# Performance work log

Hardware: AMD Instinct MI355X
Metric: run time of the kernel (lower is better)

The kernel has to match this reference:

```python
import jax, jax.numpy as jnp
import numpy as np

B, L, D, E, K, DFF = 2, 2048, 1024, 8, 2, 4096


def setup_inputs() -> dict:
    key = jax.random.key(0)
    kx, kr, kg, ku, kd = jax.random.split(key, 5)
    scale = 0.02
    return {
        "x": jax.random.normal(kx, (B, L, D), dtype=jnp.float32),
        "Wr": jax.random.normal(kr, (E, D), dtype=jnp.float32) * scale,   # router: logits = x @ Wr.T
        "Wg": jax.random.normal(kg, (E, DFF, D), dtype=jnp.float32) * scale,  # gate proj per expert
        "Wu": jax.random.normal(ku, (E, DFF, D), dtype=jnp.float32) * scale,  # up proj per expert
        "Wd": jax.random.normal(kd, (E, D, DFF), dtype=jnp.float32) * scale,  # down proj per expert
    }


def reference(x, Wr, Wg, Wu, Wd):
    Bb, Ll, Dd = x.shape
    T = Bb * Ll
    xt = x.reshape(T, Dd)                                   # [T, D]
    logits = jnp.einsum("td,ed->te", xt, Wr)                # router logits [T, E]
    scores = jax.nn.softmax(logits, axis=-1)
    k_scores, k_ids = jax.lax.top_k(scores, K)              # [T, K]
    eps = jnp.finfo(x.dtype).eps
    k_w = k_scores / (k_scores.sum(axis=-1, keepdims=True) + eps)  # renormalized top-k weights
    # combine[t, e] = sum_k k_w[t, k] * (k_ids[t, k] == e)
    combine = jnp.sum(jax.nn.one_hot(k_ids, E, dtype=x.dtype) * k_w[..., None], axis=1)  # [T, E]
    # GluMLP per expert, computed densely over all tokens (reference form)
    g = jnp.einsum("td,efd->etf", xt, Wg)                   # [E, T, DFF]
    u = jnp.einsum("td,efd->etf", xt, Wu)                   # [E, T, DFF]
    h = jax.nn.relu(g) * u
    out_e = jnp.einsum("etf,edf->etd", h, Wd)               # [E, T, D]
    out = jnp.einsum("te,etd->td", combine, out_e)          # weighted combine [T, D]
    return out.reshape(Bb, Ll, Dd)
```

## Files before the change

### kernel.cpp

```cpp
#include <hip/hip_runtime.h>
#include <hip/hip_bf16.h>

#define Tt 4096
#define Dd 1024
#define Ee 8
#define Kk 2
#define Ff 4096

using f32x4  = __attribute__((ext_vector_type(4))) float;
using bf16x8 = __attribute__((ext_vector_type(8))) short;

__device__ __forceinline__ unsigned short f2bf(float f) {
    union { float fp; unsigned int u; } v; v.fp = f;
    unsigned int u = v.u;
    return (unsigned short)((u + 0x7FFFu + ((u >> 16) & 1u)) >> 16);
}

__device__ __forceinline__ void gl16(const void* g, void* l) {
    __builtin_amdgcn_global_load_lds(
        (const __attribute__((address_space(1))) void*)g,
        (__attribute__((address_space(3))) void*)l, 16, 0, 0);
}

__global__ void router_kernel(const float* __restrict__ x, const float* __restrict__ Wr,
                              int* __restrict__ ids, float* __restrict__ wts,
                              int* __restrict__ counts, unsigned short* __restrict__ xb) {
    const int t = blockIdx.x;
    const int lane = threadIdx.x;
    const float* xr = x + (size_t)t * Dd + lane * 16;
    float xv[16];
#pragma unroll
    for (int i = 0; i < 4; ++i) *(float4*)(xv + 4 * i) = *(const float4*)(xr + 4 * i);
    uint4 o0, o1;
    o0.x = (unsigned)f2bf(xv[0])  | ((unsigned)f2bf(xv[1])  << 16);
    o0.y = (unsigned)f2bf(xv[2])  | ((unsigned)f2bf(xv[3])  << 16);
    o0.z = (unsigned)f2bf(xv[4])  | ((unsigned)f2bf(xv[5])  << 16);
    o0.w = (unsigned)f2bf(xv[6])  | ((unsigned)f2bf(xv[7])  << 16);
    o1.x = (unsigned)f2bf(xv[8])  | ((unsigned)f2bf(xv[9])  << 16);
    o1.y = (unsigned)f2bf(xv[10]) | ((unsigned)f2bf(xv[11]) << 16);
    o1.z = (unsigned)f2bf(xv[12]) | ((unsigned)f2bf(xv[13]) << 16);
    o1.w = (unsigned)f2bf(xv[14]) | ((unsigned)f2bf(xv[15]) << 16);
    unsigned short* xo = xb + (size_t)t * Dd + lane * 16;
    *(uint4*)(xo) = o0;
    *(uint4*)(xo + 8) = o1;

    double dot[Ee];
#pragma unroll
    for (int e = 0; e < Ee; ++e) {
        const float* wr = Wr + e * Dd + lane * 16;
        double s = 0.0;
#pragma unroll
        for (int i = 0; i < 16; ++i) s += (double)xv[i] * (double)wr[i];
        dot[e] = s;
    }
#pragma unroll
    for (int off = 32; off >= 1; off >>= 1) {
#pragma unroll
        for (int e = 0; e < Ee; ++e) dot[e] += __shfl_xor(dot[e], off, 64);
    }
    if (lane == 0) {
        float lg[Ee];
#pragma unroll
        for (int e = 0; e < Ee; ++e) lg[e] = (float)dot[e];
        float m = lg[0];
        for (int e = 1; e < Ee; ++e) m = fmaxf(m, lg[e]);
        float ex[Ee]; float sum = 0.f;
        for (int e = 0; e < Ee; ++e) { ex[e] = expf(lg[e] - m); sum += ex[e]; }
        float s0 = -1.f, s1 = -1.f; int i0 = 0, i1 = 0;
        for (int e = 0; e < Ee; ++e) {
            float s = ex[e];
            if (s > s0)      { s1 = s0; i1 = i0; s0 = s; i0 = e; }
            else if (s > s1) { s1 = s; i1 = e; }
        }
        float inv = 1.f / sum;
        float sc0 = s0 * inv, sc1 = s1 * inv;
        float den = sc0 + sc1 + 1.1920929e-7f;
        ids[2 * t] = i0; ids[2 * t + 1] = i1;
        wts[2 * t] = sc0 / den; wts[2 * t + 1] = sc1 / den;
        atomicAdd(&counts[i0], 1);
        atomicAdd(&counts[i1], 1);
    }
}

__global__ void cvt_wgu(const float* __restrict__ Wg, const float* __restrict__ Wu,
                        unsigned short* __restrict__ Wgu) {
    size_t tid = (size_t)blockIdx.x * blockDim.x + threadIdx.x;
    size_t row = tid >> 7;
    int dc  = (int)(tid & 127);
    int e   = (int)(row >> 13);
    int j   = (int)(row & 8191);
    int fg = j >> 5, s = (j >> 4) & 1, fi = j & 15;
    int f  = fg * 16 + fi;
    const float* src = (s ? Wu : Wg) + ((size_t)e * Ff + f) * Dd + dc * 8;
    float4 a = *(const float4*)(src);
    float4 b = *(const float4*)(src + 4);
    uint4 o;
    o.x = (unsigned)f2bf(a.x) | ((unsigned)f2bf(a.y) << 16);
    o.y = (unsigned)f2bf(a.z) | ((unsigned)f2bf(a.w) << 16);
    o.z = (unsigned)f2bf(b.x) | ((unsigned)f2bf(b.y) << 16);
    o.w = (unsigned)f2bf(b.z) | ((unsigned)f2bf(b.w) << 16);
    *(uint4*)(Wgu + row * Dd + dc * 8) = o;
}

__global__ void scan_kernel(const int* __restrict__ counts, int* __restrict__ cursor,
                            int* __restrict__ eoff) {
    if (threadIdx.x == 0) {
        int acc = 0;
        for (int e = 0; e < Ee; ++e) { eoff[e] = acc; cursor[e] = acc; acc += counts[e]; }
        eoff[Ee] = acc;
    }
}

__global__ void scatter_kernel(const int* __restrict__ ids,
                               int* __restrict__ cursor, int* __restrict__ rows) {
    int t = blockIdx.x * blockDim.x + threadIdx.x;
    if (t >= Tt) return;
#pragma unroll
    for (int k = 0; k < Kk; ++k) {
        int e = ids[2 * t + k];
        int pos = atomicAdd(&cursor[e], 1);
        rows[pos] = 2 * t + k;
    }
}


#define MFMA_BF16(a, b, c) __builtin_amdgcn_mfma_f32_16x16x32_bf16(a, b, c, 0, 0, 0)

template<bool G2>
__device__ __forceinline__ void gemm_body(unsigned short* Ls,
                                          const unsigned short* __restrict__ Abase,
                                          const unsigned short* __restrict__ Bbase,
                                          const int* __restrict__ eoff,
                                          const int* __restrict__ rows,
                                          unsigned short* __restrict__ H,
                                          float* __restrict__ partial) {
    constexpr int KLEN  = G2 ? Ff : Dd;
    constexpr int NT    = (G2 ? 2048 : 1024) / 64;
    constexpr int MT    = G2 ? 128 : 256;
    constexpr int MFR   = MT / 32;
    constexpr int AISS  = MT / 64;
    constexpr int AH0   = AISS / 2;
    constexpr int ABUFU = MT * 64;
    constexpr int BBASE = 2 * ABUFU;
    const int e   = blockIdx.z;
    const int off = eoff[e];
    const int ne  = eoff[e + 1] - off;
    const int by  = blockIdx.y;
    const int my  = G2 ? (by >> 1) : by;
    const int sK  = G2 ? (by & 1) : 0;
    const int koff = sK * 2048;
    const int m0  = my * MT;
    if (m0 >= ne) return;
    const int n0  = blockIdx.x * 256;

    const int tid  = threadIdx.x;
    const int lane = tid & 63;
    const int w    = tid >> 6;
    const int wr   = w >> 2;
    const int wc   = w & 3;
    const int lr   = lane & 15;
    const int lc   = lane >> 4;

    const int sr = lane >> 3;
    const int cA = (lane & 7) ^ sr;
    int asrc[AISS];
#pragma unroll
    for (int j = 0; j < AISS; ++j) {
        int rr = m0 + j * 64 + w * 8 + sr;
        if (rr > ne - 1) rr = ne - 1;
        asrc[j] = (G2 ? (off + rr) : (rows[off + rr] >> 1)) * KLEN + cA * 8;
    }
    const unsigned short* Bp = Bbase + (size_t)e * (G2 ? (size_t)Dd * Ff : (size_t)8192 * Dd);
    int bsrc[4];
#pragma unroll
    for (int qq = 0; qq < 4; ++qq) {
        int rN = n0 + qq * 64 + w * 8 + sr;
        bsrc[qq] = rN * KLEN + cA * 8;
    }

    auto STAGE_A = [&](int T, int half) {
        const int bo_ = (T & 1) * ABUFU; const int kt_ = koff + T * 64;
        if (half == 0) {
#pragma unroll
            for (int j = 0; j < AH0; ++j)
                gl16(Abase + asrc[j] + kt_, Ls + bo_ + j * 4096 + w * 512);
        } else {
#pragma unroll
            for (int j = AH0; j < AISS; ++j)
                gl16(Abase + asrc[j] + kt_, Ls + bo_ + j * 4096 + w * 512);
        }
    };
    auto STAGE_B = [&](int T, int Hh) {
        const int bo_ = BBASE + (T & 1) * 16384; const int kt_ = koff + T * 64;
        gl16(Bp + bsrc[2 * Hh]     + kt_, Ls + bo_ + (2 * Hh)     * 4096 + w * 512);
        gl16(Bp + bsrc[2 * Hh + 1] + kt_, Ls + bo_ + (2 * Hh + 1) * 4096 + w * 512);
    };

#define WAIT_STEADY() do { if constexpr (G2) { asm volatile("s_waitcnt vmcnt(2)" ::: "memory"); } \
                           else              { asm volatile("s_waitcnt vmcnt(4)" ::: "memory"); } } while (0)

    const int ccx0 = ((0 * 4 + lc) ^ (lr & 7)) * 8;
    const int ccx1 = ((1 * 4 + lc) ^ (lr & 7)) * 8;
    const int aB = (wr * (MT / 2)) * 64 + lr * 64;
    const int bB = BBASE + wc * 4096 + lr * 64;

    f32x4 acc[MFR][4];
#pragma unroll
    for (int m = 0; m < MFR; ++m)
#pragma unroll
        for (int n = 0; n < 4; ++n) acc[m][n] = (f32x4){0.f, 0.f, 0.f, 0.f};

    STAGE_A(0, 0); STAGE_A(0, 1); STAGE_B(0, 0); STAGE_B(0, 1);
    STAGE_A(1, 0); STAGE_A(1, 1);
    WAIT_STEADY();
    __builtin_amdgcn_sched_barrier(0);
    __builtin_amdgcn_s_barrier();

    bf16x8 a0[MFR], a1[MFR], b0[4], b1[4];

    for (int t = 0; t < NT; ++t) {
        const int abo = (t & 1) * ABUFU;
        const int bbo = (t & 1) * 16384;
#pragma unroll
        for (int m = 0; m < MFR; ++m) a0[m] = *(const bf16x8*)(Ls + abo + aB + m * 1024 + ccx0);
#pragma unroll
        for (int n = 0; n < 4; ++n) b0[n] = *(const bf16x8*)(Ls + bbo + bB + n * 1024 + ccx0);
        if (t + 1 < NT) STAGE_B(t + 1, 0);
        __builtin_amdgcn_s_barrier();
        asm volatile("s_waitcnt lgkmcnt(0)" ::: "memory");
        __builtin_amdgcn_sched_barrier(0);
        __builtin_amdgcn_s_setprio(1);
#pragma unroll
        for (int m = 0; m < MFR; ++m) {
            acc[m][0] = MFMA_BF16(a0[m], b0[0], acc[m][0]);
            acc[m][1] = MFMA_BF16(a0[m], b0[1], acc[m][1]);
        }
        __builtin_amdgcn_s_setprio(0);
        __builtin_amdgcn_s_barrier();
#pragma unroll
        for (int m = 0; m < MFR; ++m) a1[m] = *(const bf16x8*)(Ls + abo + aB + m * 1024 + ccx1);
        if (t + 1 < NT) STAGE_B(t + 1, 1);
        __builtin_amdgcn_s_barrier();
        __builtin_amdgcn_s_setprio(1);
#pragma unroll
        for (int m = 0; m < MFR; ++m) {
            acc[m][2] = MFMA_BF16(a0[m], b0[2], acc[m][2]);
            acc[m][3] = MFMA_BF16(a0[m], b0[3], acc[m][3]);
        }
        __builtin_amdgcn_s_setprio(0);
        asm volatile("s_waitcnt lgkmcnt(0)" ::: "memory");
        __builtin_amdgcn_sched_barrier(0);
        __builtin_amdgcn_s_barrier();
#pragma unroll
        for (int n = 0; n < 4; ++n) b1[n] = *(const bf16x8*)(Ls + bbo + bB + n * 1024 + ccx1);
        if (t + 2 < NT) STAGE_A(t + 2, 0);
        __builtin_amdgcn_s_barrier();
        asm volatile("s_waitcnt lgkmcnt(0)" ::: "memory");
        __builtin_amdgcn_sched_barrier(0);
        __builtin_amdgcn_s_setprio(1);
#pragma unroll
        for (int m = 0; m < MFR; ++m) {
            acc[m][0] = MFMA_BF16(a1[m], b1[0], acc[m][0]);
            acc[m][1] = MFMA_BF16(a1[m], b1[1], acc[m][1]);
        }
        __builtin_amdgcn_s_setprio(0);
        __builtin_amdgcn_s_barrier();
        if (t + 2 < NT) STAGE_A(t + 2, 1);
        __builtin_amdgcn_s_setprio(1);
#pragma unroll
        for (int m = 0; m < MFR; ++m) {
            acc[m][2] = MFMA_BF16(a1[m], b1[2], acc[m][2]);
            acc[m][3] = MFMA_BF16(a1[m], b1[3], acc[m][3]);
        }
        __builtin_amdgcn_s_setprio(0);
        if (t + 2 < NT) { WAIT_STEADY(); }
        else            { asm volatile("s_waitcnt vmcnt(0)" ::: "memory"); }
        __builtin_amdgcn_sched_barrier(0);
        __builtin_amdgcn_s_barrier();
    }

    if constexpr (!G2) {
        const int fg16 = ((n0 + wc * 64) >> 5) * 16 + lr;
#pragma unroll
        for (int m = 0; m < MFR; ++m) {
            const int itok = m0 + wr * (MT / 2) + m * 16 + lc * 4;
#pragma unroll
            for (int r = 0; r < 4; ++r) {
                const int i = itok + r;
                if (i < ne) {
                    unsigned short* hp = H + (size_t)(off + i) * Ff;
#pragma unroll
                    for (int np = 0; np < 2; ++np) {
                        const float g = acc[m][2 * np][r];
                        const float u = acc[m][2 * np + 1][r];
                        hp[fg16 + np * 16] = f2bf(fmaxf(g, 0.f) * u);
                    }
                }
            }
        }
    } else {
        const int dbase = n0 + wc * 64;
#pragma unroll
        for (int m = 0; m < MFR; ++m) {
            const int ib = m0 + wr * (MT / 2) + m * 16 + lc * 4;
#pragma unroll
            for (int r = 0; r < 4; ++r) {
                const int i = ib + r;
                if (i < ne) {
                    const int tr = rows[off + i];
                    float* op = partial + ((size_t)sK * 8192 + tr) * Dd + dbase + lr;
#pragma unroll
                    for (int n = 0; n < 4; ++n) op[n * 16] = acc[m][n][r];
                }
            }
        }
    }
#undef WAIT_STEADY
}

__global__ __launch_bounds__(512, 1)
void g1_moe(const unsigned short* __restrict__ xb, const unsigned short* __restrict__ Wgu,
            const int* __restrict__ eoff, const int* __restrict__ rows,
            unsigned short* __restrict__ H,
            const float* __restrict__ Wd, unsigned short* __restrict__ Wdb) {
    __shared__ __align__(16) unsigned short Ls[65536];
    gemm_body<false>(Ls, xb, Wgu, eoff, rows, H, nullptr);
    const int fb = blockIdx.x + gridDim.x * (blockIdx.y + gridDim.y * blockIdx.z);
    const size_t base = (size_t)fb * 8192;
#pragma unroll
    for (int it = 0; it < 2; ++it) {
        const size_t i = base + (size_t)it * 4096 + threadIdx.x * 8;
        float4 a = *(const float4*)(Wd + i);
        float4 b = *(const float4*)(Wd + i + 4);
        uint4 o;
        o.x = (unsigned)f2bf(a.x) | ((unsigned)f2bf(a.y) << 16);
        o.y = (unsigned)f2bf(a.z) | ((unsigned)f2bf(a.w) << 16);
        o.z = (unsigned)f2bf(b.x) | ((unsigned)f2bf(b.y) << 16);
        o.w = (unsigned)f2bf(b.z) | ((unsigned)f2bf(b.w) << 16);
        *(uint4*)(Wdb + i) = o;
    }
}

__global__ __launch_bounds__(512, 1)
void g2_moe(const unsigned short* __restrict__ H, const unsigned short* __restrict__ Wdb,
            const int* __restrict__ eoff, const int* __restrict__ rows,
            float* __restrict__ partial) {
    __shared__ __align__(16) unsigned short Ls[49152];
    gemm_body<true>(Ls, H, Wdb, eoff, rows, nullptr, partial);
}

__global__ void reduce_kernel(const float* __restrict__ P, const float* __restrict__ wts,
                              float* __restrict__ out) {
    const size_t idx = (size_t)blockIdx.x * blockDim.x + threadIdx.x;
    const size_t t  = idx >> 8;
    const int   dq  = (int)(idx & 255);
    const float w0 = wts[2 * t], w1 = wts[2 * t + 1];
    const float4* p00 = (const float4*)(P + (2 * t)        * Dd) + dq;
    const float4* p01 = (const float4*)(P + (2 * t + 1)    * Dd) + dq;
    const float4* p10 = (const float4*)(P + ((size_t)8192 + 2 * t)     * Dd) + dq;
    const float4* p11 = (const float4*)(P + ((size_t)8192 + 2 * t + 1) * Dd) + dq;
    float4 a = *p00, b = *p01, c = *p10, d = *p11;
    float4 o;
    o.x = w0 * (a.x + c.x) + w1 * (b.x + d.x);
    o.y = w0 * (a.y + c.y) + w1 * (b.y + d.y);
    o.z = w0 * (a.z + c.z) + w1 * (b.z + d.z);
    o.w = w0 * (a.w + c.w) + w1 * (b.w + d.w);
    ((float4*)(out + t * Dd))[dq] = o;
}

extern "C" void kernel_launch(void* const* d_in, const int* in_sizes, int n_in,
                              void* d_out, int out_size, void* d_ws, size_t ws_size,
                              hipStream_t stream) {
    const float* x  = (const float*)d_in[0];
    const float* Wr = (const float*)d_in[1];
    const float* Wg = (const float*)d_in[2];
    const float* Wu = (const float*)d_in[3];
    const float* Wd = (const float*)d_in[4];
    float* out = (float*)d_out;
    char* ws = (char*)d_ws;

    const size_t WELEM    = (size_t)Ee * Ff * Dd;
    const size_t OFF_IDS  = 256;
    const size_t OFF_WTS  = OFF_IDS  + (size_t)Tt * 2 * 4;
    const size_t OFF_ROWS = OFF_WTS  + (size_t)Tt * 2 * 4;
    const size_t OFF_ROWW = OFF_ROWS + (size_t)Tt * Kk * 4;
    const size_t OFF_XB   = OFF_ROWW + (size_t)Tt * Kk * 4;
    const size_t OFF_H    = OFF_XB   + (size_t)Tt * Dd * 2;
    const size_t OFF_WGU  = OFF_H    + (size_t)Tt * Kk * Ff * 2;
    const size_t OFF_WD   = OFF_WGU  + WELEM * 2 * 2;
    const size_t NEED     = OFF_WD   + WELEM * 2;
    if (ws_size < NEED) return;

    int* counts = (int*)ws;
    int* cursor = (int*)(ws + 32);
    int* eoff   = (int*)(ws + 64);
    int* ids    = (int*)(ws + OFF_IDS);
    float* wts  = (float*)(ws + OFF_WTS);
    int* rows   = (int*)(ws + OFF_ROWS);
    unsigned short* xb  = (unsigned short*)(ws + OFF_XB);
    unsigned short* H   = (unsigned short*)(ws + OFF_H);
    unsigned short* Wgu = (unsigned short*)(ws + OFF_WGU);
    unsigned short* Wdb = (unsigned short*)(ws + OFF_WD);
    float* partial = (float*)(ws + OFF_WGU);

    hipMemsetAsync(ws, 0, 256, stream);

    router_kernel  <<<Tt, 64, 0, stream>>>(x, Wr, ids, wts, counts, xb);
    scan_kernel    <<<1, 64, 0, stream>>>(counts, cursor, eoff);
    scatter_kernel <<<Tt / 256, 256, 0, stream>>>(ids, cursor, rows);

    cvt_wgu        <<<32768, 256, 0, stream>>>(Wg, Wu, Wgu);

    g1_moe <<<dim3(2 * Ff / 256, Tt / 256, Ee), 512, 0, stream>>>(
        xb, Wgu, eoff, rows, H, Wd, Wdb);
    g2_moe <<<dim3(Dd / 256, 20, Ee), 512, 0, stream>>>(
        H, Wdb, eoff, rows, partial);

    reduce_kernel  <<<(Tt * Dd / 4) / 256, 256, 0, stream>>>(partial, wts, out);
}
```

Before: 494.8 us.

## Narrow g2 N-tile to 128 and store split-K partials as bf16

The down-projection GEMM now uses a 128-wide N tile instead of 256. That doubles the grid in x and cuts LDS to 64KB, giving more blocks to fill the CUs. The split-K partial sums are written as bf16 instead of fp32, which halves the partial write and reduce traffic; the reduce kernel is rewritten to read bf16x8 vectors. The cost is less B-operand reuse per block and extra rounding error from storing the partial results in bf16.

```diff
diff --git a/kernel.cpp b/kernel.cpp
--- a/kernel.cpp
+++ b/kernel.cpp
@@ -14,6 +14,10 @@
     union { float fp; unsigned int u; } v; v.fp = f;
     unsigned int u = v.u;
     return (unsigned short)((u + 0x7FFFu + ((u >> 16) & 1u)) >> 16);
+}
+
+__device__ __forceinline__ float b2f(unsigned short u) {
+    union { float f; unsigned int i; } v; v.i = (unsigned)u << 16; return v.f;
 }
 
 __device__ __forceinline__ void gl16(const void* g, void* l) {
@@ -133,14 +137,19 @@
                                           const int* __restrict__ eoff,
                                           const int* __restrict__ rows,
                                           unsigned short* __restrict__ H,
-                                          float* __restrict__ partial) {
+                                          unsigned short* __restrict__ partial) {
     constexpr int KLEN  = G2 ? Ff : Dd;
     constexpr int NT    = (G2 ? 2048 : 1024) / 64;
     constexpr int MT    = G2 ? 128 : 256;
+    constexpr int BN    = G2 ? 128 : 256;
     constexpr int MFR   = MT / 32;
+    constexpr int NF    = BN / 64;
     constexpr int AISS  = MT / 64;
+    constexpr int BISS  = BN / 64;
     constexpr int AH0   = AISS / 2;
+    constexpr int BH0   = BISS / 2;
     constexpr int ABUFU = MT * 64;
+    constexpr int BBUFU = BN * 64;
     constexpr int BBASE = 2 * ABUFU;
     const int e   = blockIdx.z;
     const int off = eoff[e];
@@ -151,7 +160,7 @@
     const int koff = sK * 2048;
     const int m0  = my * MT;
     if (m0 >= ne) return;
-    const int n0  = blockIdx.x * 256;
+    const int n0  = blockIdx.x * BN;
 
     const int tid  = threadIdx.x;
     const int lane = tid & 63;
@@ -171,11 +180,11 @@
         asrc[j] = (G2 ? (off + rr) : (rows[off + rr] >> 1)) * KLEN + cA * 8;
     }
     const unsigned short* Bp = Bbase + (size_t)e * (G2 ? (size_t)Dd * Ff : (size_t)8192 * Dd);
-    int bsrc[4];
-#pragma unroll
-    for (int qq = 0; qq < 4; ++qq) {
-        int rN = n0 + qq * 64 + w * 8 + sr;
-        bsrc[qq] = rN * KLEN + cA * 8;
+    int bsrc[BISS];
+#pragma unroll
+    for (int j = 0; j < BISS; ++j) {
+        int rN = n0 + j * 64 + w * 8 + sr;
+        bsrc[j] = rN * KLEN + cA * 8;
     }
 
     auto STAGE_A = [&](int T, int half) {
@@ -190,10 +199,17 @@
                 gl16(Abase + asrc[j] + kt_, Ls + bo_ + j * 4096 + w * 512);
         }
     };
-    auto STAGE_B = [&](int T, int Hh) {
-        const int bo_ = BBASE + (T & 1) * 16384; const int kt_ = koff + T * 64;
-        gl16(Bp + bsrc[2 * Hh]     + kt_, Ls + bo_ + (2 * Hh)     * 4096 + w * 512);
-        gl16(Bp + bsrc[2 * Hh + 1] + kt_, Ls + bo_ + (2 * Hh + 1) * 4096 + w * 512);
+    auto STAGE_B = [&](int T, int half) {
+        const int bo_ = BBASE + (T & 1) * BBUFU; const int kt_ = koff + T * 64;
+        if (half == 0) {
+#pragma unroll
+            for (int j = 0; j < BH0; ++j)
+                gl16(Bp + bsrc[j] + kt_, Ls + bo_ + j * 4096 + w * 512);
+        } else {
+#pragma unroll
+            for (int j = BH0; j < BISS; ++j)
+                gl16(Bp + bsrc[j] + kt_, Ls + bo_ + j * 4096 + w * 512);
+        }
     };
 
 #define WAIT_STEADY() do { if constexpr (G2) { asm volatile("s_waitcnt vmcnt(2)" ::: "memory"); } \
@@ -202,13 +218,13 @@
     const int ccx0 = ((0 * 4 + lc) ^ (lr & 7)) * 8;
     const int ccx1 = ((1 * 4 + lc) ^ (lr & 7)) * 8;
     const int aB = (wr * (MT / 2)) * 64 + lr * 64;
-    const int bB = BBASE + wc * 4096 + lr * 64;
-
-    f32x4 acc[MFR][4];
+    const int bB = BBASE + (wc * (BN / 4)) * 64 + lr * 64;
+
+    f32x4 acc[MFR][NF];
 #pragma unroll
     for (int m = 0; m < MFR; ++m)
 #pragma unroll
-        for (int n = 0; n < 4; ++n) acc[m][n] = (f32x4){0.f, 0.f, 0.f, 0.f};
+        for (int n = 0; n < NF; ++n) acc[m][n] = (f32x4){0.f, 0.f, 0.f, 0.f};
 
     STAGE_A(0, 0); STAGE_A(0, 1); STAGE_B(0, 0); STAGE_B(0, 1);
     STAGE_A(1, 0); STAGE_A(1, 1);
@@ -216,25 +232,25 @@
     __builtin_amdgcn_sched_barrier(0);
     __builtin_amdgcn_s_barrier();
 
-    bf16x8 a0[MFR], a1[MFR], b0[4], b1[4];
+    bf16x8 a0[MFR], a1[MFR], b0[NF], b1[NF];
 
     for (int t = 0; t < NT; ++t) {
         const int abo = (t & 1) * ABUFU;
-        const int bbo = (t & 1) * 16384;
+        const int bbo = (t & 1) * BBUFU;
 #pragma unroll
         for (int m = 0; m < MFR; ++m) a0[m] = *(const bf16x8*)(Ls + abo + aB + m * 1024 + ccx0);
 #pragma unroll
-        for (int n = 0; n < 4; ++n) b0[n] = *(const bf16x8*)(Ls + bbo + bB + n * 1024 + ccx0);
+        for (int n = 0; n < NF; ++n) b0[n] = *(const bf16x8*)(Ls + bbo + bB + n * 1024 + ccx0);
         if (t + 1 < NT) STAGE_B(t + 1, 0);
         __builtin_amdgcn_s_barrier();
         asm volatile("s_waitcnt lgkmcnt(0)" ::: "memory");
         __builtin_amdgcn_sched_barrier(0);
         __builtin_amdgcn_s_setprio(1);
 #pragma unroll
-        for (int m = 0; m < MFR; ++m) {
-            acc[m][0] = MFMA_BF16(a0[m], b0[0], acc[m][0]);
-            acc[m][1] = MFMA_BF16(a0[m], b0[1], acc[m][1]);
-        }
+        for (int m = 0; m < MFR; ++m)
+#pragma unroll
+            for (int n = 0; n < NF / 2; ++n)
+                acc[m][n] = MFMA_BF16(a0[m], b0[n], acc[m][n]);
         __builtin_amdgcn_s_setprio(0);
         __builtin_amdgcn_s_barrier();
 #pragma unroll
@@ -243,35 +259,35 @@
         __builtin_amdgcn_s_barrier();
         __builtin_amdgcn_s_setprio(1);
 #pragma unroll
-        for (int m = 0; m < MFR; ++m) {
-            acc[m][2] = MFMA_BF16(a0[m], b0[2], acc[m][2]);
-            acc[m][3] = MFMA_BF16(a0[m], b0[3], acc[m][3]);
-        }
+        for (int m = 0; m < MFR; ++m)
+#pragma unroll
+            for (int n = NF / 2; n < NF; ++n)
+                acc[m][n] = MFMA_BF16(a0[m], b0[n], acc[m][n]);
         __builtin_amdgcn_s_setprio(0);
         asm volatile("s_waitcnt lgkmcnt(0)" ::: "memory");
         __builtin_amdgcn_sched_barrier(0);
         __builtin_amdgcn_s_barrier();
 #pragma unroll
-        for (int n = 0; n < 4; ++n) b1[n] = *(const bf16x8*)(Ls + bbo + bB + n * 1024 + ccx1);
+        for (int n = 0; n < NF; ++n) b1[n] = *(const bf16x8*)(Ls + bbo + bB + n * 1024 + ccx1);
         if (t + 2 < NT) STAGE_A(t + 2, 0);
         __builtin_amdgcn_s_barrier();
         asm volatile("s_waitcnt lgkmcnt(0)" ::: "memory");
         __builtin_amdgcn_sched_barrier(0);
         __builtin_amdgcn_s_setprio(1);
 #pragma unroll
-        for (int m = 0; m < MFR; ++m) {
-            acc[m][0] = MFMA_BF16(a1[m], b1[0], acc[m][0]);
-            acc[m][1] = MFMA_BF16(a1[m], b1[1], acc[m][1]);
-        }
+        for (int m = 0; m < MFR; ++m)
+#pragma unroll
+            for (int n = 0; n < NF / 2; ++n)
+                acc[m][n] = MFMA_BF16(a1[m], b1[n], acc[m][n]);
         __builtin_amdgcn_s_setprio(0);
         __builtin_amdgcn_s_barrier();
         if (t + 2 < NT) STAGE_A(t + 2, 1);
         __builtin_amdgcn_s_setprio(1);
 #pragma unroll
-        for (int m = 0; m < MFR; ++m) {
-            acc[m][2] = MFMA_BF16(a1[m], b1[2], acc[m][2]);
-            acc[m][3] = MFMA_BF16(a1[m], b1[3], acc[m][3]);
-        }
+        for (int m = 0; m < MFR; ++m)
+#pragma unroll
+            for (int n = NF / 2; n < NF; ++n)
+                acc[m][n] = MFMA_BF16(a1[m], b1[n], acc[m][n]);
         __builtin_amdgcn_s_setprio(0);
         if (t + 2 < NT) { WAIT_STEADY(); }
         else            { asm volatile("s_waitcnt vmcnt(0)" ::: "memory"); }
@@ -299,7 +315,7 @@
             }
         }
     } else {
-        const int dbase = n0 + wc * 64;
+        const int dbase = n0 + wc * (BN / 4);
 #pragma unroll
         for (int m = 0; m < MFR; ++m) {
             const int ib = m0 + wr * (MT / 2) + m * 16 + lc * 4;
@@ -308,9 +324,9 @@
                 const int i = ib + r;
                 if (i < ne) {
                     const int tr = rows[off + i];
-                    float* op = partial + ((size_t)sK * 8192 + tr) * Dd + dbase + lr;
-#pragma unroll
-                    for (int n = 0; n < 4; ++n) op[n * 16] = acc[m][n][r];
+                    unsigned short* op = partial + ((size_t)sK * 8192 + tr) * Dd + dbase + lr;
+#pragma unroll
+                    for (int n = 0; n < NF; ++n) op[n * 16] = f2bf(acc[m][n][r]);
                 }
             }
         }
@@ -344,28 +360,33 @@
 __global__ __launch_bounds__(512, 1)
 void g2_moe(const unsigned short* __restrict__ H, const unsigned short* __restrict__ Wdb,
             const int* __restrict__ eoff, const int* __restrict__ rows,
-            float* __restrict__ partial) {
-    __shared__ __align__(16) unsigned short Ls[49152];
+            unsigned short* __restrict__ partial) {
+    __shared__ __align__(16) unsigned short Ls[32768];
     gemm_body<true>(Ls, H, Wdb, eoff, rows, nullptr, partial);
 }
 
-__global__ void reduce_kernel(const float* __restrict__ P, const float* __restrict__ wts,
+__global__ void reduce_kernel(const unsigned short* __restrict__ P, const float* __restrict__ wts,
                               float* __restrict__ out) {
     const size_t idx = (size_t)blockIdx.x * blockDim.x + threadIdx.x;
-    const size_t t  = idx >> 8;
-    const int   dq  = (int)(idx & 255);
+    const size_t t  = idx >> 7;
+    const int   dq  = (int)(idx & 127);
     const float w0 = wts[2 * t], w1 = wts[2 * t + 1];
-    const float4* p00 = (const float4*)(P + (2 * t)        * Dd) + dq;
-    const float4* p01 = (const float4*)(P + (2 * t + 1)    * Dd) + dq;
-    const float4* p10 = (const float4*)(P + ((size_t)8192 + 2 * t)     * Dd) + dq;
-    const float4* p11 = (const float4*)(P + ((size_t)8192 + 2 * t + 1) * Dd) + dq;
-    float4 a = *p00, b = *p01, c = *p10, d = *p11;
-    float4 o;
-    o.x = w0 * (a.x + c.x) + w1 * (b.x + d.x);
-    o.y = w0 * (a.y + c.y) + w1 * (b.y + d.y);
-    o.z = w0 * (a.z + c.z) + w1 * (b.z + d.z);
-    o.w = w0 * (a.w + c.w) + w1 * (b.w + d.w);
-    ((float4*)(out + t * Dd))[dq] = o;
+    const unsigned short* p00 = P + ((size_t)(2 * t))            * Dd + dq * 8;
+    const unsigned short* p01 = P + ((size_t)(2 * t + 1))        * Dd + dq * 8;
+    const unsigned short* p10 = P + ((size_t)8192 + 2 * t)       * Dd + dq * 8;
+    const unsigned short* p11 = P + ((size_t)8192 + 2 * t + 1)   * Dd + dq * 8;
+    bf16x8 a = *(const bf16x8*)p00;
+    bf16x8 b = *(const bf16x8*)p01;
+    bf16x8 c = *(const bf16x8*)p10;
+    bf16x8 d = *(const bf16x8*)p11;
+    float o[8];
+#pragma unroll
+    for (int j = 0; j < 8; ++j)
+        o[j] = w0 * (b2f((unsigned short)a[j]) + b2f((unsigned short)c[j]))
+             + w1 * (b2f((unsigned short)b[j]) + b2f((unsigned short)d[j]));
+    float* op = out + t * Dd + dq * 8;
+    *(float4*)(op)     = (float4){o[0], o[1], o[2], o[3]};
+    *(float4*)(op + 4) = (float4){o[4], o[5], o[6], o[7]};
 }
 
 extern "C" void kernel_launch(void* const* d_in, const int* in_sizes, int n_in,
@@ -401,7 +422,7 @@
     unsigned short* H   = (unsigned short*)(ws + OFF_H);
     unsigned short* Wgu = (unsigned short*)(ws + OFF_WGU);
     unsigned short* Wdb = (unsigned short*)(ws + OFF_WD);
-    float* partial = (float*)(ws + OFF_WGU);
+    unsigned short* partial = (unsigned short*)(ws + OFF_WGU);
 
     hipMemsetAsync(ws, 0, 256, stream);
 
@@ -413,8 +434,8 @@
 
     g1_moe <<<dim3(2 * Ff / 256, Tt / 256, Ee), 512, 0, stream>>>(
         xb, Wgu, eoff, rows, H, Wd, Wdb);
-    g2_moe <<<dim3(Dd / 256, 20, Ee), 512, 0, stream>>>(
+    g2_moe <<<dim3(Dd / 128, 20, Ee), 512, 0, stream>>>(
         H, Wdb, eoff, rows, partial);
 
-    reduce_kernel  <<<(Tt * Dd / 4) / 256, 256, 0, stream>>>(partial, wts, out);
-}
+    reduce_kernel  <<<(Tt * Dd / 8) / 256, 256, 0, stream>>>(partial, wts, out);
+}
```

Result: no change. 496.2 us (+0.3%).
